# Kernel optimization log

Measured on AMD Instinct MI355X. Metric: run time of the kernel, lower is better.

Reference implementation:

```python
import jax, jax.numpy as jnp
import numpy as np

# SamplesLoss(loss='sinkhorn', p=1, blur=0.05): entropic regularization eps = blur**p = 0.05,
# debiased Sinkhorn divergence S(a,b) = OT(a,b) - 0.5*OT(a,a) - 0.5*OT(b,b).
EPS = 0.05
N_ITER = 50
N_POINTS = 32


def _cost(X, Y):
    # p=1 cost: Euclidean distance. X:[B,N,D] Y:[B,M,D] -> [B,N,M]
    d2 = jnp.sum((X[:, :, None, :] - Y[:, None, :, :]) ** 2, axis=-1)
    return jnp.sqrt(d2 + 1e-12)


def _ot(X, Y):
    # log-domain Sinkhorn with uniform weights; returns dual cost <mu,f>+<nu,g> per batch.
    B, N, _ = X.shape
    M = Y.shape[1]
    C = _cost(X, Y)  # [B,N,M]
    log_mu = jnp.full((B, N), -np.log(N), C.dtype)
    log_nu = jnp.full((B, M), -np.log(M), C.dtype)

    def body(carry, _):
        f, g = carry
        f = -EPS * jax.nn.logsumexp((g[:, None, :] - C) / EPS + log_nu[:, None, :], axis=2)
        g = -EPS * jax.nn.logsumexp((f[:, :, None] - C) / EPS + log_mu[:, :, None], axis=1)
        return (f, g), None

    init = (jnp.zeros((B, N), C.dtype), jnp.zeros((B, M), C.dtype))
    (f, g), _ = jax.lax.scan(body, init, None, length=N_ITER)
    return jnp.mean(f, axis=-1) + jnp.mean(g, axis=-1)  # uniform weights => mean


def _sinkhorn_div(X, Y):
    return _ot(X, Y) - 0.5 * _ot(X, X) - 0.5 * _ot(Y, Y)


def _encode(x, W, edge_index):
    # simple 1-layer GCN-style encoder: linear + mean neighbor aggregation + self, ReLU
    h = x @ W  # [n_nodes, emb_dim]
    src, dst = edge_index[0], edge_index[1]
    n = x.shape[0]
    agg = jax.ops.segment_sum(h[src], dst, num_segments=n)
    deg = jax.ops.segment_sum(jnp.ones(src.shape, h.dtype), dst, num_segments=n)
    return jax.nn.relu(h + agg / jnp.maximum(deg, 1.0)[:, None])


def setup_inputs() -> dict:
    key = jax.random.key(0)
    k1, k2, k3, k4, k5 = jax.random.split(key, 5)
    n_nodes, d_feat, emb_dim = 50000, 128, 256
    n_edges, n_pairs = 800000, 8192
    x = jax.random.normal(k1, (n_nodes, d_feat), jnp.float32)
    W = jax.random.normal(k2, (d_feat, emb_dim), jnp.float32) / np.sqrt(d_feat)
    edge_index = jax.random.randint(k3, (2, n_edges), 0, n_nodes, jnp.int64)
    pairs = jax.random.randint(k4, (2, n_pairs), 0, n_nodes, jnp.int64)
    graph_dist = jax.random.uniform(k5, (n_pairs,), jnp.float32, 1.0, 5.0)
    return {"x": x, "W": W, "edge_index": edge_index, "pairs": pairs,
            "graph_dist": graph_dist}


def reference(x, W, edge_index, pairs, graph_dist):
    z = _encode(x, W, edge_index)                       # [n_nodes, emb_dim]
    B = pairs.shape[1]
    Xa = z[pairs[0]].reshape(B, N_POINTS, -1)           # [B, n_points, space_dim]
    Xb = z[pairs[1]].reshape(B, N_POINTS, -1)
    distance = _sinkhorn_div(Xa, Xb)                    # = -score_pairs
    distortion = jnp.abs(distance - graph_dist) / graph_dist
    return jnp.mean(distortion)
```

## Files before the change

kernel.cpp:

```cpp
#include <hip/hip_runtime.h>

#define N_NODES 50000
#define N_EDGES 800000
#define N_PAIRS 8192
#define N_SLOTS (2 * N_PAIRS)
#define CAP     64

#define INV_EPS   20.0f
#define LOG2E_F   1.4426950408889634f
#define LN2_F     0.6931471805599453f
#define LN32_F    3.4657359027997265f
#define EPS_F     0.05f

typedef float f2 __attribute__((ext_vector_type(2)));

__global__ void k_mark(const int* __restrict__ pairs, int* __restrict__ flags) {
    int t = blockIdx.x * 256 + threadIdx.x;
    if (t < N_SLOTS) flags[pairs[t]] = 1;
}

__global__ __launch_bounds__(256) void k_scatter(
        const int* __restrict__ eidx, const int* __restrict__ flags,
        int* __restrict__ cnt, int* __restrict__ bucket) {
    int t = blockIdx.x * 256 + threadIdx.x;
    int dst = eidx[N_EDGES + t];
    if (!flags[dst]) return;
    int pos = atomicAdd(&cnt[dst], 1);
    if (pos < CAP) bucket[dst * CAP + pos] = eidx[t];
}

__global__ __launch_bounds__(256) void k_gemm(
        const int* __restrict__ pairs, const float* __restrict__ x,
        const int* __restrict__ cnt, const int* __restrict__ bucket,
        const float* __restrict__ W, float* __restrict__ Z) {
    __shared__ __align__(16) float Us[16 * 128];
    int sbase = blockIdx.x * 16;
    int t = threadIdx.x;
    int wave = t >> 6, lane = t & 63;

    #pragma unroll
    for (int rr = 0; rr < 4; ++rr) {
        int r = wave * 4 + rr;
        int node = pairs[sbase + r];
        int n = cnt[node];
        int m = (n < CAP) ? n : CAP;
        const int* bk = bucket + node * CAP;
        float ax = 0.0f, ay = 0.0f;
        int k = 0;
        for (; k + 4 <= m; k += 4) {
            int s0 = bk[k], s1 = bk[k + 1], s2 = bk[k + 2], s3 = bk[k + 3];
            float2 v0 = *(const float2*)(x + (size_t)s0 * 128 + lane * 2);
            float2 v1 = *(const float2*)(x + (size_t)s1 * 128 + lane * 2);
            float2 v2 = *(const float2*)(x + (size_t)s2 * 128 + lane * 2);
            float2 v3 = *(const float2*)(x + (size_t)s3 * 128 + lane * 2);
            ax += (v0.x + v1.x) + (v2.x + v3.x);
            ay += (v0.y + v1.y) + (v2.y + v3.y);
        }
        for (; k < m; ++k) {
            int s0 = bk[k];
            float2 v0 = *(const float2*)(x + (size_t)s0 * 128 + lane * 2);
            ax += v0.x;
            ay += v0.y;
        }
        float rdeg = 1.0f / fmaxf((float)n, 1.0f);
        float2 xv = *(const float2*)(x + (size_t)node * 128 + lane * 2);
        float2 o;
        o.x = fmaf(ax, rdeg, xv.x);
        o.y = fmaf(ay, rdeg, xv.y);
        *(float2*)(Us + r * 128 + lane * 2) = o;
    }
    __syncthreads();

    int jq = t & 63;
    int rq = t >> 6;
    float acc[4][4] = {};
    const float4* Wv = (const float4*)W;

    for (int k4 = 0; k4 < 32; ++k4) {
        float4 wv[4];
        #pragma unroll
        for (int i = 0; i < 4; ++i) wv[i] = Wv[(size_t)(k4 * 4 + i) * 64 + jq];
        #pragma unroll
        for (int r = 0; r < 4; ++r) {
            float4 uv = *(const float4*)(Us + (rq * 4 + r) * 128 + k4 * 4);
            float uk0 = uv.x, uk1 = uv.y, uk2 = uv.z, uk3 = uv.w;
            acc[r][0] = fmaf(uk0, wv[0].x, acc[r][0]);
            acc[r][1] = fmaf(uk0, wv[0].y, acc[r][1]);
            acc[r][2] = fmaf(uk0, wv[0].z, acc[r][2]);
            acc[r][3] = fmaf(uk0, wv[0].w, acc[r][3]);
            acc[r][0] = fmaf(uk1, wv[1].x, acc[r][0]);
            acc[r][1] = fmaf(uk1, wv[1].y, acc[r][1]);
            acc[r][2] = fmaf(uk1, wv[1].z, acc[r][2]);
            acc[r][3] = fmaf(uk1, wv[1].w, acc[r][3]);
            acc[r][0] = fmaf(uk2, wv[2].x, acc[r][0]);
            acc[r][1] = fmaf(uk2, wv[2].y, acc[r][1]);
            acc[r][2] = fmaf(uk2, wv[2].z, acc[r][2]);
            acc[r][3] = fmaf(uk2, wv[2].w, acc[r][3]);
            acc[r][0] = fmaf(uk3, wv[3].x, acc[r][0]);
            acc[r][1] = fmaf(uk3, wv[3].y, acc[r][1]);
            acc[r][2] = fmaf(uk3, wv[3].z, acc[r][2]);
            acc[r][3] = fmaf(uk3, wv[3].w, acc[r][3]);
        }
    }

    #pragma unroll
    for (int r = 0; r < 4; ++r) {
        float4 o;
        o.x = fmaxf(acc[r][0], 0.0f);
        o.y = fmaxf(acc[r][1], 0.0f);
        o.z = fmaxf(acc[r][2], 0.0f);
        o.w = fmaxf(acc[r][3], 0.0f);
        *(float4*)(Z + (size_t)(sbase + rq * 4 + r) * 256 + jq * 4) = o;
    }
}

__global__ __launch_bounds__(128) void k_sinkhorn(
        const float* __restrict__ Z, float* __restrict__ dist) {
    __shared__ __align__(16) float smem[2][640];

    int w = threadIdx.x >> 6;
    int lane = threadIdx.x & 63;
    const float CSCALE = -INV_EPS * LOG2E_F;
    const float CBIAS  = -LN32_F * LOG2E_F;

    if (blockIdx.x >= 4096) {
        float* sX = &smem[w][0];
        float* sY = &smem[w][256];
        float* sf = &smem[w][512];
        float* sg = &smem[w][544];
        float* su = &smem[w][576];
        float* sv = &smem[w][608];

        int b = (blockIdx.x - 4096) * 2 + w;
        int sx = b, sy = N_PAIRS + b;

        *(float4*)(&sX[lane * 4]) = ((const float4*)(Z + (size_t)sx * 256))[lane];
        *(float4*)(&sY[lane * 4]) = ((const float4*)(Z + (size_t)sy * 256))[lane];
        sg[lane & 31] = 0.0f;

        int i_r = lane & 31, jh = lane >> 5;
        int j_c = lane & 31, ih = lane >> 5;

        f2 CrowV[8], CcolV[8];
        {
            const f2* xp = (const f2*)(&sX[i_r * 8]);
            f2 x0 = xp[0], x1 = xp[1], x2 = xp[2], x3 = xp[3];
            #pragma unroll
            for (int t = 0; t < 16; ++t) {
                int j = jh * 16 + t;
                const f2* yp = (const f2*)(&sY[j * 8]);
                f2 d, s2;
                d = x0 - yp[0]; s2 = d * d;
                d = x1 - yp[1]; s2 = __builtin_elementwise_fma(d, d, s2);
                d = x2 - yp[2]; s2 = __builtin_elementwise_fma(d, d, s2);
                d = x3 - yp[3]; s2 = __builtin_elementwise_fma(d, d, s2);
                float d2 = s2.x + s2.y + 1e-12f;
                CrowV[t >> 1][t & 1] = fmaf(__builtin_amdgcn_sqrtf(d2), CSCALE, CBIAS);
            }
            const f2* yp = (const f2*)(&sY[j_c * 8]);
            f2 y0 = yp[0], y1 = yp[1], y2 = yp[2], y3 = yp[3];
            #pragma unroll
            for (int t = 0; t < 16; ++t) {
                int i = ih * 16 + t;
                const f2* qp = (const f2*)(&sX[i * 8]);
                f2 d, s2;
                d = qp[0] - y0; s2 = d * d;
                d = qp[1] - y1; s2 = __builtin_elementwise_fma(d, d, s2);
                d = qp[2] - y2; s2 = __builtin_elementwise_fma(d, d, s2);
                d = qp[3] - y3; s2 = __builtin_elementwise_fma(d, d, s2);
                float d2 = s2.x + s2.y + 1e-12f;
                CcolV[t >> 1][t & 1] = fmaf(__builtin_amdgcn_sqrtf(d2), CSCALE, CBIAS);
            }
        }

        float ft = 0.0f, gt = 0.0f;

        #pragma unroll 1
        for (int it = 0; it < 2; ++it) {
            {
                const float4* gp = (const float4*)(&sg[jh * 16]);
                float4 G0 = gp[0], G1 = gp[1], G2 = gp[2], G3 = gp[3];
                f2 gv[8] = {f2{G0.x, G0.y}, f2{G0.z, G0.w}, f2{G1.x, G1.y}, f2{G1.z, G1.w},
                            f2{G2.x, G2.y}, f2{G2.z, G2.w}, f2{G3.x, G3.y}, f2{G3.z, G3.w}};
                f2 val[8], m2 = f2{-1e30f, -1e30f};
                #pragma unroll
                for (int t2 = 0; t2 < 8; ++t2) {
                    val[t2] = gv[t2] + CrowV[t2];
                    m2 = __builtin_elementwise_max(m2, val[t2]);
                }
                float m = fmaxf(m2.x, m2.y);
                m = fmaxf(m, __shfl_xor(m, 32));
                f2 mm = f2{m, m};
                float s0 = 0.0f, s1 = 0.0f;
                #pragma unroll
                for (int t2 = 0; t2 < 8; ++t2) {
                    f2 e = val[t2] - mm;
                    s0 += __builtin_amdgcn_exp2f(e.x);
                    s1 += __builtin_amdgcn_exp2f(e.y);
                }
                float s = s0 + s1;
                s += __shfl_xor(s, 32);
                ft = -(m + __builtin_amdgcn_logf(s));
            }
            sf[lane & 31] = ft;
            {
                const float4* fp = (const float4*)(&sf[ih * 16]);
                float4 F0 = fp[0], F1 = fp[1], F2 = fp[2], F3 = fp[3];
                f2 fv[8] = {f2{F0.x, F0.y}, f2{F0.z, F0.w}, f2{F1.x, F1.y}, f2{F1.z, F1.w},
                            f2{F2.x, F2.y}, f2{F2.z, F2.w}, f2{F3.x, F3.y}, f2{F3.z, F3.w}};
                f2 val[8], m2 = f2{-1e30f, -1e30f};
                #pragma unroll
                for (int t2 = 0; t2 < 8; ++t2) {
                    val[t2] = fv[t2] + CcolV[t2];
                    m2 = __builtin_elementwise_max(m2, val[t2]);
                }
                float m = fmaxf(m2.x, m2.y);
                m = fmaxf(m, __shfl_xor(m, 32));
                f2 mm = f2{m, m};
                float s0 = 0.0f, s1 = 0.0f;
                #pragma unroll
                for (int t2 = 0; t2 < 8; ++t2) {
                    f2 e = val[t2] - mm;
                    s0 += __builtin_amdgcn_exp2f(e.x);
                    s1 += __builtin_amdgcn_exp2f(e.y);
                }
                float s = s0 + s1;
                s += __shfl_xor(s, 32);
                gt = -(m + __builtin_amdgcn_logf(s));
            }
            sg[lane & 31] = gt;
        }

        f2 KR2[8], KC2[8];
        float ureg = 1.0f, vreg = 1.0f;

        auto absorb = [&]() {
            const float4* gp = (const float4*)(&sg[jh * 16]);
            float4 G0 = gp[0], G1 = gp[1], G2 = gp[2], G3 = gp[3];
            f2 gv[8] = {f2{G0.x, G0.y}, f2{G0.z, G0.w}, f2{G1.x, G1.y}, f2{G1.z, G1.w},
                        f2{G2.x, G2.y}, f2{G2.z, G2.w}, f2{G3.x, G3.y}, f2{G3.z, G3.w}};
            f2 ftv = f2{ft, ft};
            #pragma unroll
            for (int t2 = 0; t2 < 8; ++t2) {
                f2 a = (gv[t2] + CrowV[t2]) + ftv;
                KR2[t2].x = __builtin_amdgcn_exp2f(a.x);
                KR2[t2].y = __builtin_amdgcn_exp2f(a.y);
            }
            const float4* fp = (const float4*)(&sf[ih * 16]);
            float4 F0 = fp[0], F1 = fp[1], F2 = fp[2], F3 = fp[3];
            f2 fv[8] = {f2{F0.x, F0.y}, f2{F0.z, F0.w}, f2{F1.x, F1.y}, f2{F1.z, F1.w},
                        f2{F2.x, F2.y}, f2{F2.z, F2.w}, f2{F3.x, F3.y}, f2{F3.z, F3.w}};
            f2 gtv = f2{gt, gt};
            #pragma unroll
            for (int t2 = 0; t2 < 8; ++t2) {
                f2 a = (fv[t2] + CcolV[t2]) + gtv;
                KC2[t2].x = __builtin_amdgcn_exp2f(a.x);
                KC2[t2].y = __builtin_amdgcn_exp2f(a.y);
            }
            sv[lane & 31] = 1.0f;
            ureg = 1.0f;
            vreg = 1.0f;
        };

        const int blens[5] = {6, 6, 12, 12, 12};
        absorb();
        #pragma unroll 1
        for (int blk = 0; blk < 5; ++blk) {
            int L = blens[blk];
            #pragma unroll 2
            for (int s6 = 0; s6 < L; ++s6) {
                {
                    const float4* vp = (const float4*)(&sv[jh * 16]);
                    float4 A0 = vp[0], A1 = vp[1], A2 = vp[2], A3 = vp[3];
                    f2 acc0 = KR2[0] * f2{A0.x, A0.y};
                    f2 acc1 = KR2[1] * f2{A0.z, A0.w};
                    acc0 = __builtin_elementwise_fma(KR2[2], f2{A1.x, A1.y}, acc0);
                    acc1 = __builtin_elementwise_fma(KR2[3], f2{A1.z, A1.w}, acc1);
                    acc0 = __builtin_elementwise_fma(KR2[4], f2{A2.x, A2.y}, acc0);
                    acc1 = __builtin_elementwise_fma(KR2[5], f2{A2.z, A2.w}, acc1);
                    acc0 = __builtin_elementwise_fma(KR2[6], f2{A3.x, A3.y}, acc0);
                    acc1 = __builtin_elementwise_fma(KR2[7], f2{A3.z, A3.w}, acc1);
                    f2 a = acc0 + acc1;
                    float S = a.x + a.y;
                    S += __shfl_xor(S, 32);
                    ureg = __builtin_amdgcn_rcpf(S);
                }
                su[lane & 31] = ureg;
                {
                    const float4* up = (const float4*)(&su[ih * 16]);
                    float4 A0 = up[0], A1 = up[1], A2 = up[2], A3 = up[3];
                    f2 acc0 = KC2[0] * f2{A0.x, A0.y};
                    f2 acc1 = KC2[1] * f2{A0.z, A0.w};
                    acc0 = __builtin_elementwise_fma(KC2[2], f2{A1.x, A1.y}, acc0);
                    acc1 = __builtin_elementwise_fma(KC2[3], f2{A1.z, A1.w}, acc1);
                    acc0 = __builtin_elementwise_fma(KC2[4], f2{A2.x, A2.y}, acc0);
                    acc1 = __builtin_elementwise_fma(KC2[5], f2{A2.z, A2.w}, acc1);
                    acc0 = __builtin_elementwise_fma(KC2[6], f2{A3.x, A3.y}, acc0);
                    acc1 = __builtin_elementwise_fma(KC2[7], f2{A3.z, A3.w}, acc1);
                    f2 a = acc0 + acc1;
                    float T = a.x + a.y;
                    T += __shfl_xor(T, 32);
                    vreg = __builtin_amdgcn_rcpf(T);
                }
                sv[lane & 31] = vreg;
            }
            if (blk < 4) {
                ft += __builtin_amdgcn_logf(ureg);
                gt += __builtin_amdgcn_logf(vreg);
                sf[lane & 31] = ft;
                sg[lane & 31] = gt;
                absorb();
            }
        }
        ft += __builtin_amdgcn_logf(ureg);
        gt += __builtin_amdgcn_logf(vreg);

        float v = ft + gt;
        #pragma unroll
        for (int off = 32; off > 0; off >>= 1) v += __shfl_xor(v, off);
        if (lane == 0) {
            float cost = v * (EPS_F * LN2_F / 64.0f);
            unsafeAtomicAdd(&dist[b], cost);
        }
    } else {
        int h = lane >> 5, i = lane & 31;
        int q = (i >> 4) & 1;
        int ip = i ^ 16;
        int P = blockIdx.x * 2 + w;
        int src = h ? (N_PAIRS + P) : P;

        float* sP  = &smem[w][h * 256];
        float* swv = &smem[w][512];
        float* spv = &smem[w][576];

        {
            const float4* zp = (const float4*)(Z + (size_t)src * 256);
            *(float4*)(&sP[i * 8])     = zp[i * 2];
            *(float4*)(&sP[i * 8 + 4]) = zp[i * 2 + 1];
        }

        f2 CA[8], CB[8];
        {
            const f2* xp = (const f2*)(&sP[i * 8]);
            f2 x0 = xp[0], x1 = xp[1], x2 = xp[2], x3 = xp[3];
            const f2* bp = (const f2*)(&sP[ip * 8]);
            f2 b0 = bp[0], b1 = bp[1], b2 = bp[2], b3 = bp[3];
            #pragma unroll
            for (int t = 0; t < 16; ++t) {
                int j = q * 16 + t;
                const f2* yp = (const f2*)(&sP[j * 8]);
                f2 y0 = yp[0], y1 = yp[1], y2 = yp[2], y3 = yp[3];
                f2 d, s2;
                d = x0 - y0; s2 = d * d;
                d = x1 - y1; s2 = __builtin_elementwise_fma(d, d, s2);
                d = x2 - y2; s2 = __builtin_elementwise_fma(d, d, s2);
                d = x3 - y3; s2 = __builtin_elementwise_fma(d, d, s2);
                float d2 = s2.x + s2.y + 1e-12f;
                CA[t >> 1][t & 1] = fmaf(__builtin_amdgcn_sqrtf(d2), CSCALE, CBIAS);
                d = b0 - y0; s2 = d * d;
                d = b1 - y1; s2 = __builtin_elementwise_fma(d, d, s2);
                d = b2 - y2; s2 = __builtin_elementwise_fma(d, d, s2);
                d = b3 - y3; s2 = __builtin_elementwise_fma(d, d, s2);
                float e2 = s2.x + s2.y + 1e-12f;
                CB[t >> 1][t & 1] = fmaf(__builtin_amdgcn_sqrtf(e2), CSCALE, CBIAS);
            }
        }

        float pp = 0.0f, E = 1.0f, wcur = 1.0f, wprev = 1.0f;
        f2 KA[8], KB[8];
        #pragma unroll
        for (int t = 0; t < 8; ++t) {
            KA[t].x = __builtin_amdgcn_exp2f(CA[t].x);
            KA[t].y = __builtin_amdgcn_exp2f(CA[t].y);
            KB[t].x = __builtin_amdgcn_exp2f(CB[t].x);
            KB[t].y = __builtin_amdgcn_exp2f(CB[t].y);
        }
        swv[lane] = 1.0f;

        const int blens[9] = {4, 12, 12, 12, 12, 12, 12, 12, 12};
        #pragma unroll 1
        for (int blk = 0; blk < 9; ++blk) {
            int L = blens[blk];
            #pragma unroll 2
            for (int s = 0; s < L; ++s) {
                const float4* wp = (const float4*)(&swv[h * 32 + q * 16]);
                float4 A0 = wp[0], A1 = wp[1], A2 = wp[2], A3 = wp[3];
                f2 aA0 = KA[0] * f2{A0.x, A0.y};
                f2 aA1 = KA[1] * f2{A0.z, A0.w};
                f2 aB0 = KB[0] * f2{A0.x, A0.y};
                f2 aB1 = KB[1] * f2{A0.z, A0.w};
                aA0 = __builtin_elementwise_fma(KA[2], f2{A1.x, A1.y}, aA0);
                aA1 = __builtin_elementwise_fma(KA[3], f2{A1.z, A1.w}, aA1);
                aB0 = __builtin_elementwise_fma(KB[2], f2{A1.x, A1.y}, aB0);
                aB1 = __builtin_elementwise_fma(KB[3], f2{A1.z, A1.w}, aB1);
                aA0 = __builtin_elementwise_fma(KA[4], f2{A2.x, A2.y}, aA0);
                aA1 = __builtin_elementwise_fma(KA[5], f2{A2.z, A2.w}, aA1);
                aB0 = __builtin_elementwise_fma(KB[4], f2{A2.x, A2.y}, aB0);
                aB1 = __builtin_elementwise_fma(KB[5], f2{A2.z, A2.w}, aB1);
                aA0 = __builtin_elementwise_fma(KA[6], f2{A3.x, A3.y}, aA0);
                aA1 = __builtin_elementwise_fma(KA[7], f2{A3.z, A3.w}, aA1);
                aB0 = __builtin_elementwise_fma(KB[6], f2{A3.x, A3.y}, aB0);
                aB1 = __builtin_elementwise_fma(KB[7], f2{A3.z, A3.w}, aB1);
                f2 aa = aA0 + aA1;
                f2 bb = aB0 + aB1;
                float pa = aa.x + aa.y;
                float pb = bb.x + bb.y;
                float other = __shfl_xor(pb, 16);
                float S = pa + other;
                wprev = wcur;
                wcur = __builtin_amdgcn_rcpf(S) * E;
                swv[h * 32 + i] = wcur;
            }
            if (blk < 8) {
                pp += __builtin_amdgcn_logf(wcur);
                spv[lane] = pp;
                const float4* pv = (const float4*)(&spv[h * 32 + q * 16]);
                float4 P0 = pv[0], P1 = pv[1], P2 = pv[2], P3 = pv[3];
                f2 pj[8] = {f2{P0.x,P0.y}, f2{P0.z,P0.w}, f2{P1.x,P1.y}, f2{P1.z,P1.w},
                            f2{P2.x,P2.y}, f2{P2.z,P2.w}, f2{P3.x,P3.y}, f2{P3.z,P3.w}};
                #pragma unroll
                for (int t = 0; t < 8; ++t) {
                    f2 a = pj[t] + CA[t];
                    KA[t].x = __builtin_amdgcn_exp2f(a.x);
                    KA[t].y = __builtin_amdgcn_exp2f(a.y);
                    f2 c = pj[t] + CB[t];
                    KB[t].x = __builtin_amdgcn_exp2f(c.x);
                    KB[t].y = __builtin_amdgcn_exp2f(c.y);
                }
                E = __builtin_amdgcn_exp2f(-pp);
                wcur = 1.0f;
                swv[lane] = 1.0f;
            }
        }

        float zsum = 2.0f * pp + __builtin_amdgcn_logf(wprev)
                   + __builtin_amdgcn_logf(wcur);
        #pragma unroll
        for (int off = 16; off > 0; off >>= 1) zsum += __shfl_xor(zsum, off);
        if (i == 0) {
            float cost = zsum * (EPS_F * LN2_F / 32.0f);
            unsafeAtomicAdd(&dist[P], -0.5f * cost);
        }
    }
}

__global__ void k_finalize(const float* __restrict__ dist,
                           const float* __restrict__ gd, float* __restrict__ out) {
    __shared__ float red[256];
    float s = 0.0f;
    for (int i = threadIdx.x; i < N_PAIRS; i += 256) {
        float g = gd[i];
        s += fabsf(dist[i] - g) / g;
    }
    red[threadIdx.x] = s;
    __syncthreads();
    for (int o = 128; o > 0; o >>= 1) {
        if (threadIdx.x < o) red[threadIdx.x] += red[threadIdx.x + o];
        __syncthreads();
    }
    if (threadIdx.x == 0) out[0] = red[0] * (1.0f / N_PAIRS);
}

extern "C" void kernel_launch(void* const* d_in, const int* in_sizes, int n_in,
                              void* d_out, int out_size, void* d_ws, size_t ws_size,
                              hipStream_t stream) {
    const float* x    = (const float*)d_in[0];
    const float* W    = (const float*)d_in[1];
    const int*   eidx = (const int*)d_in[2];
    const int*   pair = (const int*)d_in[3];
    const float* gd   = (const float*)d_in[4];

    char* ws = (char*)d_ws;
    size_t off = 0;
    int*   cnt    = (int*)  (ws + off); off += (size_t)N_NODES * 4;
    int*   flags  = (int*)  (ws + off); off += (size_t)N_NODES * 4;
    float* dist   = (float*)(ws + off); off += (size_t)N_PAIRS * 4;
    size_t zero_bytes = off;
    int*   bucket = (int*)  (ws + off); off += (size_t)N_NODES * CAP * 4;
    float* Z      = (float*)(ws + off); off += (size_t)N_SLOTS * 256 * 4;

    hipMemsetAsync(d_ws, 0, zero_bytes, stream);
    k_mark    <<<(N_SLOTS + 255) / 256, 256, 0, stream>>>(pair, flags);
    k_scatter <<<N_EDGES / 256, 256, 0, stream>>>(eidx, flags, cnt, bucket);
    k_gemm    <<<N_SLOTS / 16, 256, 0, stream>>>(pair, x, cnt, bucket, W, Z);
    k_sinkhorn<<<8192, 128, 0, stream>>>(Z, dist);
    k_finalize<<<1, 256, 0, stream>>>(dist, gd, (float*)d_out);
}
```

Baseline: 252.0 us.

## Interleave two Sinkhorn problems per wavefront and rescale kernels incrementally

Result: slower. 263.2 us (+4.4%).

```diff
diff --git a/kernel.cpp b/kernel.cpp
--- a/kernel.cpp
+++ b/kernel.cpp
@@ -114,233 +114,34 @@
     }
 }
 
-__global__ __launch_bounds__(128) void k_sinkhorn(
+__global__ __launch_bounds__(128, 4) void k_sinkhorn(
         const float* __restrict__ Z, float* __restrict__ dist) {
-    __shared__ __align__(16) float smem[2][640];
+    __shared__ __align__(16) float smem[2][1280];
 
     int w = threadIdx.x >> 6;
     int lane = threadIdx.x & 63;
+    float* S = &smem[w][0];
     const float CSCALE = -INV_EPS * LOG2E_F;
     const float CBIAS  = -LN32_F * LOG2E_F;
 
-    if (blockIdx.x >= 4096) {
-        float* sX = &smem[w][0];
-        float* sY = &smem[w][256];
-        float* sf = &smem[w][512];
-        float* sg = &smem[w][544];
-        float* su = &smem[w][576];
-        float* sv = &smem[w][608];
-
-        int b = (blockIdx.x - 4096) * 2 + w;
-        int sx = b, sy = N_PAIRS + b;
-
-        *(float4*)(&sX[lane * 4]) = ((const float4*)(Z + (size_t)sx * 256))[lane];
-        *(float4*)(&sY[lane * 4]) = ((const float4*)(Z + (size_t)sy * 256))[lane];
-        sg[lane & 31] = 0.0f;
-
-        int i_r = lane & 31, jh = lane >> 5;
-        int j_c = lane & 31, ih = lane >> 5;
-
-        f2 CrowV[8], CcolV[8];
-        {
-            const f2* xp = (const f2*)(&sX[i_r * 8]);
-            f2 x0 = xp[0], x1 = xp[1], x2 = xp[2], x3 = xp[3];
-            #pragma unroll
-            for (int t = 0; t < 16; ++t) {
-                int j = jh * 16 + t;
-                const f2* yp = (const f2*)(&sY[j * 8]);
-                f2 d, s2;
-                d = x0 - yp[0]; s2 = d * d;
-                d = x1 - yp[1]; s2 = __builtin_elementwise_fma(d, d, s2);
-                d = x2 - yp[2]; s2 = __builtin_elementwise_fma(d, d, s2);
-                d = x3 - yp[3]; s2 = __builtin_elementwise_fma(d, d, s2);
-                float d2 = s2.x + s2.y + 1e-12f;
-                CrowV[t >> 1][t & 1] = fmaf(__builtin_amdgcn_sqrtf(d2), CSCALE, CBIAS);
-            }
-            const f2* yp = (const f2*)(&sY[j_c * 8]);
-            f2 y0 = yp[0], y1 = yp[1], y2 = yp[2], y3 = yp[3];
-            #pragma unroll
-            for (int t = 0; t < 16; ++t) {
-                int i = ih * 16 + t;
-                const f2* qp = (const f2*)(&sX[i * 8]);
-                f2 d, s2;
-                d = qp[0] - y0; s2 = d * d;
-                d = qp[1] - y1; s2 = __builtin_elementwise_fma(d, d, s2);
-                d = qp[2] - y2; s2 = __builtin_elementwise_fma(d, d, s2);
-                d = qp[3] - y3; s2 = __builtin_elementwise_fma(d, d, s2);
-                float d2 = s2.x + s2.y + 1e-12f;
-                CcolV[t >> 1][t & 1] = fmaf(__builtin_amdgcn_sqrtf(d2), CSCALE, CBIAS);
-            }
-        }
-
-        float ft = 0.0f, gt = 0.0f;
-
-        #pragma unroll 1
-        for (int it = 0; it < 2; ++it) {
-            {
-                const float4* gp = (const float4*)(&sg[jh * 16]);
-                float4 G0 = gp[0], G1 = gp[1], G2 = gp[2], G3 = gp[3];
-                f2 gv[8] = {f2{G0.x, G0.y}, f2{G0.z, G0.w}, f2{G1.x, G1.y}, f2{G1.z, G1.w},
-                            f2{G2.x, G2.y}, f2{G2.z, G2.w}, f2{G3.x, G3.y}, f2{G3.z, G3.w}};
-                f2 val[8], m2 = f2{-1e30f, -1e30f};
-                #pragma unroll
-                for (int t2 = 0; t2 < 8; ++t2) {
-                    val[t2] = gv[t2] + CrowV[t2];
-                    m2 = __builtin_elementwise_max(m2, val[t2]);
-                }
-                float m = fmaxf(m2.x, m2.y);
-                m = fmaxf(m, __shfl_xor(m, 32));
-                f2 mm = f2{m, m};
-                float s0 = 0.0f, s1 = 0.0f;
-                #pragma unroll
-                for (int t2 = 0; t2 < 8; ++t2) {
-                    f2 e = val[t2] - mm;
-                    s0 += __builtin_amdgcn_exp2f(e.x);
-                    s1 += __builtin_amdgcn_exp2f(e.y);
-                }
-                float s = s0 + s1;
-                s += __shfl_xor(s, 32);
-                ft = -(m + __builtin_amdgcn_logf(s));
-            }
-            sf[lane & 31] = ft;
-            {
-                const float4* fp = (const float4*)(&sf[ih * 16]);
-                float4 F0 = fp[0], F1 = fp[1], F2 = fp[2], F3 = fp[3];
-                f2 fv[8] = {f2{F0.x, F0.y}, f2{F0.z, F0.w}, f2{F1.x, F1.y}, f2{F1.z, F1.w},
-                            f2{F2.x, F2.y}, f2{F2.z, F2.w}, f2{F3.x, F3.y}, f2{F3.z, F3.w}};
-                f2 val[8], m2 = f2{-1e30f, -1e30f};
-                #pragma unroll
-                for (int t2 = 0; t2 < 8; ++t2) {
-                    val[t2] = fv[t2] + CcolV[t2];
-                    m2 = __builtin_elementwise_max(m2, val[t2]);
-                }
-                float m = fmaxf(m2.x, m2.y);
-                m = fmaxf(m, __shfl_xor(m, 32));
-                f2 mm = f2{m, m};
-                float s0 = 0.0f, s1 = 0.0f;
-                #pragma unroll
-                for (int t2 = 0; t2 < 8; ++t2) {
-                    f2 e = val[t2] - mm;
-                    s0 += __builtin_amdgcn_exp2f(e.x);
-                    s1 += __builtin_amdgcn_exp2f(e.y);
-                }
-                float s = s0 + s1;
-                s += __shfl_xor(s, 32);
-                gt = -(m + __builtin_amdgcn_logf(s));
-            }
-            sg[lane & 31] = gt;
-        }
-
-        f2 KR2[8], KC2[8];
-        float ureg = 1.0f, vreg = 1.0f;
-
-        auto absorb = [&]() {
-            const float4* gp = (const float4*)(&sg[jh * 16]);
-            float4 G0 = gp[0], G1 = gp[1], G2 = gp[2], G3 = gp[3];
-            f2 gv[8] = {f2{G0.x, G0.y}, f2{G0.z, G0.w}, f2{G1.x, G1.y}, f2{G1.z, G1.w},
-                        f2{G2.x, G2.y}, f2{G2.z, G2.w}, f2{G3.x, G3.y}, f2{G3.z, G3.w}};
-            f2 ftv = f2{ft, ft};
-            #pragma unroll
-            for (int t2 = 0; t2 < 8; ++t2) {
-                f2 a = (gv[t2] + CrowV[t2]) + ftv;
-                KR2[t2].x = __builtin_amdgcn_exp2f(a.x);
-                KR2[t2].y = __builtin_amdgcn_exp2f(a.y);
-            }
-            const float4* fp = (const float4*)(&sf[ih * 16]);
-            float4 F0 = fp[0], F1 = fp[1], F2 = fp[2], F3 = fp[3];
-            f2 fv[8] = {f2{F0.x, F0.y}, f2{F0.z, F0.w}, f2{F1.x, F1.y}, f2{F1.z, F1.w},
-                        f2{F2.x, F2.y}, f2{F2.z, F2.w}, f2{F3.x, F3.y}, f2{F3.z, F3.w}};
-            f2 gtv = f2{gt, gt};
-            #pragma unroll
-            for (int t2 = 0; t2 < 8; ++t2) {
-                f2 a = (fv[t2] + CcolV[t2]) + gtv;
-                KC2[t2].x = __builtin_amdgcn_exp2f(a.x);
-                KC2[t2].y = __builtin_amdgcn_exp2f(a.y);
-            }
-            sv[lane & 31] = 1.0f;
-            ureg = 1.0f;
-            vreg = 1.0f;
-        };
-
-        const int blens[5] = {6, 6, 12, 12, 12};
-        absorb();
-        #pragma unroll 1
-        for (int blk = 0; blk < 5; ++blk) {
-            int L = blens[blk];
-            #pragma unroll 2
-            for (int s6 = 0; s6 < L; ++s6) {
-                {
-                    const float4* vp = (const float4*)(&sv[jh * 16]);
-                    float4 A0 = vp[0], A1 = vp[1], A2 = vp[2], A3 = vp[3];
-                    f2 acc0 = KR2[0] * f2{A0.x, A0.y};
-                    f2 acc1 = KR2[1] * f2{A0.z, A0.w};
-                    acc0 = __builtin_elementwise_fma(KR2[2], f2{A1.x, A1.y}, acc0);
-                    acc1 = __builtin_elementwise_fma(KR2[3], f2{A1.z, A1.w}, acc1);
-                    acc0 = __builtin_elementwise_fma(KR2[4], f2{A2.x, A2.y}, acc0);
-                    acc1 = __builtin_elementwise_fma(KR2[5], f2{A2.z, A2.w}, acc1);
-                    acc0 = __builtin_elementwise_fma(KR2[6], f2{A3.x, A3.y}, acc0);
-                    acc1 = __builtin_elementwise_fma(KR2[7], f2{A3.z, A3.w}, acc1);
-                    f2 a = acc0 + acc1;
-                    float S = a.x + a.y;
-                    S += __shfl_xor(S, 32);
-                    ureg = __builtin_amdgcn_rcpf(S);
-                }
-                su[lane & 31] = ureg;
-                {
-                    const float4* up = (const float4*)(&su[ih * 16]);
-                    float4 A0 = up[0], A1 = up[1], A2 = up[2], A3 = up[3];
-                    f2 acc0 = KC2[0] * f2{A0.x, A0.y};
-                    f2 acc1 = KC2[1] * f2{A0.z, A0.w};
-                    acc0 = __builtin_elementwise_fma(KC2[2], f2{A1.x, A1.y}, acc0);
-                    acc1 = __builtin_elementwise_fma(KC2[3], f2{A1.z, A1.w}, acc1);
-                    acc0 = __builtin_elementwise_fma(KC2[4], f2{A2.x, A2.y}, acc0);
-                    acc1 = __builtin_elementwise_fma(KC2[5], f2{A2.z, A2.w}, acc1);
-                    acc0 = __builtin_elementwise_fma(KC2[6], f2{A3.x, A3.y}, acc0);
-                    acc1 = __builtin_elementwise_fma(KC2[7], f2{A3.z, A3.w}, acc1);
-                    f2 a = acc0 + acc1;
-                    float T = a.x + a.y;
-                    T += __shfl_xor(T, 32);
-                    vreg = __builtin_amdgcn_rcpf(T);
-                }
-                sv[lane & 31] = vreg;
-            }
-            if (blk < 4) {
-                ft += __builtin_amdgcn_logf(ureg);
-                gt += __builtin_amdgcn_logf(vreg);
-                sf[lane & 31] = ft;
-                sg[lane & 31] = gt;
-                absorb();
-            }
-        }
-        ft += __builtin_amdgcn_logf(ureg);
-        gt += __builtin_amdgcn_logf(vreg);
-
-        float v = ft + gt;
-        #pragma unroll
-        for (int off = 32; off > 0; off >>= 1) v += __shfl_xor(v, off);
-        if (lane == 0) {
-            float cost = v * (EPS_F * LN2_F / 64.0f);
-            unsafeAtomicAdd(&dist[b], cost);
-        }
-    } else {
+    if (blockIdx.x < 2048) {
         int h = lane >> 5, i = lane & 31;
         int q = (i >> 4) & 1;
         int ip = i ^ 16;
-        int P = blockIdx.x * 2 + w;
-        int src = h ? (N_PAIRS + P) : P;
-
-        float* sP  = &smem[w][h * 256];
-        float* swv = &smem[w][512];
-        float* spv = &smem[w][576];
-
-        {
+        int Pb = blockIdx.x * 4 + w * 2;
+
+        f2 KA[2][8], KB[2][8];
+        float pp[2] = {0.0f, 0.0f}, E[2] = {1.0f, 1.0f};
+        float wcur[2] = {1.0f, 1.0f}, wprev[2] = {1.0f, 1.0f};
+
+        #pragma unroll
+        for (int tk = 0; tk < 2; ++tk) {
+            int P = Pb + tk;
+            int src = h ? (N_PAIRS + P) : P;
+            float* sP = S + tk * 512 + h * 256;
             const float4* zp = (const float4*)(Z + (size_t)src * 256);
             *(float4*)(&sP[i * 8])     = zp[i * 2];
             *(float4*)(&sP[i * 8 + 4]) = zp[i * 2 + 1];
-        }
-
-        f2 CA[8], CB[8];
-        {
             const f2* xp = (const f2*)(&sP[i * 8]);
             f2 x0 = xp[0], x1 = xp[1], x2 = xp[2], x3 = xp[3];
             const f2* bp = (const f2*)(&sP[ip * 8]);
@@ -356,90 +157,368 @@
                 d = x2 - y2; s2 = __builtin_elementwise_fma(d, d, s2);
                 d = x3 - y3; s2 = __builtin_elementwise_fma(d, d, s2);
                 float d2 = s2.x + s2.y + 1e-12f;
-                CA[t >> 1][t & 1] = fmaf(__builtin_amdgcn_sqrtf(d2), CSCALE, CBIAS);
+                KA[tk][t >> 1][t & 1] = __builtin_amdgcn_exp2f(
+                    fmaf(__builtin_amdgcn_sqrtf(d2), CSCALE, CBIAS));
                 d = b0 - y0; s2 = d * d;
                 d = b1 - y1; s2 = __builtin_elementwise_fma(d, d, s2);
                 d = b2 - y2; s2 = __builtin_elementwise_fma(d, d, s2);
                 d = b3 - y3; s2 = __builtin_elementwise_fma(d, d, s2);
                 float e2 = s2.x + s2.y + 1e-12f;
-                CB[t >> 1][t & 1] = fmaf(__builtin_amdgcn_sqrtf(e2), CSCALE, CBIAS);
-            }
-        }
-
-        float pp = 0.0f, E = 1.0f, wcur = 1.0f, wprev = 1.0f;
-        f2 KA[8], KB[8];
-        #pragma unroll
-        for (int t = 0; t < 8; ++t) {
-            KA[t].x = __builtin_amdgcn_exp2f(CA[t].x);
-            KA[t].y = __builtin_amdgcn_exp2f(CA[t].y);
-            KB[t].x = __builtin_amdgcn_exp2f(CB[t].x);
-            KB[t].y = __builtin_amdgcn_exp2f(CB[t].y);
-        }
-        swv[lane] = 1.0f;
+                KB[tk][t >> 1][t & 1] = __builtin_amdgcn_exp2f(
+                    fmaf(__builtin_amdgcn_sqrtf(e2), CSCALE, CBIAS));
+            }
+            (S + 1024 + tk * 64)[lane] = 1.0f;
+        }
 
         const int blens[9] = {4, 12, 12, 12, 12, 12, 12, 12, 12};
         #pragma unroll 1
         for (int blk = 0; blk < 9; ++blk) {
             int L = blens[blk];
-            #pragma unroll 2
+            #pragma unroll 1
             for (int s = 0; s < L; ++s) {
-                const float4* wp = (const float4*)(&swv[h * 32 + q * 16]);
-                float4 A0 = wp[0], A1 = wp[1], A2 = wp[2], A3 = wp[3];
-                f2 aA0 = KA[0] * f2{A0.x, A0.y};
-                f2 aA1 = KA[1] * f2{A0.z, A0.w};
-                f2 aB0 = KB[0] * f2{A0.x, A0.y};
-                f2 aB1 = KB[1] * f2{A0.z, A0.w};
-                aA0 = __builtin_elementwise_fma(KA[2], f2{A1.x, A1.y}, aA0);
-                aA1 = __builtin_elementwise_fma(KA[3], f2{A1.z, A1.w}, aA1);
-                aB0 = __builtin_elementwise_fma(KB[2], f2{A1.x, A1.y}, aB0);
-                aB1 = __builtin_elementwise_fma(KB[3], f2{A1.z, A1.w}, aB1);
-                aA0 = __builtin_elementwise_fma(KA[4], f2{A2.x, A2.y}, aA0);
-                aA1 = __builtin_elementwise_fma(KA[5], f2{A2.z, A2.w}, aA1);
-                aB0 = __builtin_elementwise_fma(KB[4], f2{A2.x, A2.y}, aB0);
-                aB1 = __builtin_elementwise_fma(KB[5], f2{A2.z, A2.w}, aB1);
-                aA0 = __builtin_elementwise_fma(KA[6], f2{A3.x, A3.y}, aA0);
-                aA1 = __builtin_elementwise_fma(KA[7], f2{A3.z, A3.w}, aA1);
-                aB0 = __builtin_elementwise_fma(KB[6], f2{A3.x, A3.y}, aB0);
-                aB1 = __builtin_elementwise_fma(KB[7], f2{A3.z, A3.w}, aB1);
-                f2 aa = aA0 + aA1;
-                f2 bb = aB0 + aB1;
-                float pa = aa.x + aa.y;
-                float pb = bb.x + bb.y;
-                float other = __shfl_xor(pb, 16);
-                float S = pa + other;
-                wprev = wcur;
-                wcur = __builtin_amdgcn_rcpf(S) * E;
-                swv[h * 32 + i] = wcur;
+                #pragma unroll
+                for (int tk = 0; tk < 2; ++tk) {
+                    float* swv = S + 1024 + tk * 64;
+                    const float4* wp = (const float4*)(&swv[h * 32 + q * 16]);
+                    float4 A0 = wp[0], A1 = wp[1], A2 = wp[2], A3 = wp[3];
+                    f2 aA0 = KA[tk][0] * f2{A0.x, A0.y};
+                    f2 aA1 = KA[tk][1] * f2{A0.z, A0.w};
+                    f2 aB0 = KB[tk][0] * f2{A0.x, A0.y};
+                    f2 aB1 = KB[tk][1] * f2{A0.z, A0.w};
+                    aA0 = __builtin_elementwise_fma(KA[tk][2], f2{A1.x, A1.y}, aA0);
+                    aA1 = __builtin_elementwise_fma(KA[tk][3], f2{A1.z, A1.w}, aA1);
+                    aB0 = __builtin_elementwise_fma(KB[tk][2], f2{A1.x, A1.y}, aB0);
+                    aB1 = __builtin_elementwise_fma(KB[tk][3], f2{A1.z, A1.w}, aB1);
+                    aA0 = __builtin_elementwise_fma(KA[tk][4], f2{A2.x, A2.y}, aA0);
+                    aA1 = __builtin_elementwise_fma(KA[tk][5], f2{A2.z, A2.w}, aA1);
+                    aB0 = __builtin_elementwise_fma(KB[tk][4], f2{A2.x, A2.y}, aB0);
+                    aB1 = __builtin_elementwise_fma(KB[tk][5], f2{A2.z, A2.w}, aB1);
+                    aA0 = __builtin_elementwise_fma(KA[tk][6], f2{A3.x, A3.y}, aA0);
+                    aA1 = __builtin_elementwise_fma(KA[tk][7], f2{A3.z, A3.w}, aA1);
+                    aB0 = __builtin_elementwise_fma(KB[tk][6], f2{A3.x, A3.y}, aB0);
+                    aB1 = __builtin_elementwise_fma(KB[tk][7], f2{A3.z, A3.w}, aB1);
+                    f2 aa = aA0 + aA1;
+                    f2 bb = aB0 + aB1;
+                    float pa = aa.x + aa.y;
+                    float pb = bb.x + bb.y;
+                    float other = __shfl_xor(pb, 16);
+                    float Sv = pa + other;
+                    wprev[tk] = wcur[tk];
+                    wcur[tk] = __builtin_amdgcn_rcpf(Sv) * E[tk];
+                    swv[h * 32 + i] = wcur[tk];
+                }
             }
             if (blk < 8) {
-                pp += __builtin_amdgcn_logf(wcur);
-                spv[lane] = pp;
-                const float4* pv = (const float4*)(&spv[h * 32 + q * 16]);
-                float4 P0 = pv[0], P1 = pv[1], P2 = pv[2], P3 = pv[3];
-                f2 pj[8] = {f2{P0.x,P0.y}, f2{P0.z,P0.w}, f2{P1.x,P1.y}, f2{P1.z,P1.w},
-                            f2{P2.x,P2.y}, f2{P2.z,P2.w}, f2{P3.x,P3.y}, f2{P3.z,P3.w}};
-                #pragma unroll
-                for (int t = 0; t < 8; ++t) {
-                    f2 a = pj[t] + CA[t];
-                    KA[t].x = __builtin_amdgcn_exp2f(a.x);
-                    KA[t].y = __builtin_amdgcn_exp2f(a.y);
-                    f2 c = pj[t] + CB[t];
-                    KB[t].x = __builtin_amdgcn_exp2f(c.x);
-                    KB[t].y = __builtin_amdgcn_exp2f(c.y);
-                }
-                E = __builtin_amdgcn_exp2f(-pp);
-                wcur = 1.0f;
-                swv[lane] = 1.0f;
-            }
-        }
-
-        float zsum = 2.0f * pp + __builtin_amdgcn_logf(wprev)
-                   + __builtin_amdgcn_logf(wcur);
+                #pragma unroll
+                for (int tk = 0; tk < 2; ++tk) {
+                    float* swv = S + 1024 + tk * 64;
+                    float* sdp = S + 1152 + tk * 64;
+                    float d = __builtin_amdgcn_logf(wcur[tk]);
+                    pp[tk] += d;
+                    sdp[h * 32 + i] = d;
+                    const float4* dv = (const float4*)(&sdp[h * 32 + q * 16]);
+                    float4 D0 = dv[0], D1 = dv[1], D2 = dv[2], D3 = dv[3];
+                    float ex[16];
+                    ex[0] = __builtin_amdgcn_exp2f(D0.x);
+                    ex[1] = __builtin_amdgcn_exp2f(D0.y);
+                    ex[2] = __builtin_amdgcn_exp2f(D0.z);
+                    ex[3] = __builtin_amdgcn_exp2f(D0.w);
+                    ex[4] = __builtin_amdgcn_exp2f(D1.x);
+                    ex[5] = __builtin_amdgcn_exp2f(D1.y);
+                    ex[6] = __builtin_amdgcn_exp2f(D1.z);
+                    ex[7] = __builtin_amdgcn_exp2f(D1.w);
+                    ex[8] = __builtin_amdgcn_exp2f(D2.x);
+                    ex[9] = __builtin_amdgcn_exp2f(D2.y);
+                    ex[10] = __builtin_amdgcn_exp2f(D2.z);
+                    ex[11] = __builtin_amdgcn_exp2f(D2.w);
+                    ex[12] = __builtin_amdgcn_exp2f(D3.x);
+                    ex[13] = __builtin_amdgcn_exp2f(D3.y);
+                    ex[14] = __builtin_amdgcn_exp2f(D3.z);
+                    ex[15] = __builtin_amdgcn_exp2f(D3.w);
+                    #pragma unroll
+                    for (int t2 = 0; t2 < 8; ++t2) {
+                        f2 ee = f2{ex[2 * t2], ex[2 * t2 + 1]};
+                        KA[tk][t2] *= ee;
+                        KB[tk][t2] *= ee;
+                    }
+                    E[tk] = __builtin_amdgcn_exp2f(-pp[tk]);
+                    wcur[tk] = 1.0f;
+                    swv[lane] = 1.0f;
+                }
+            }
+        }
+
         #pragma unroll
-        for (int off = 16; off > 0; off >>= 1) zsum += __shfl_xor(zsum, off);
-        if (i == 0) {
-            float cost = zsum * (EPS_F * LN2_F / 32.0f);
-            unsafeAtomicAdd(&dist[P], -0.5f * cost);
+        for (int tk = 0; tk < 2; ++tk) {
+            float zsum = 2.0f * pp[tk] + __builtin_amdgcn_logf(wprev[tk])
+                       + __builtin_amdgcn_logf(wcur[tk]);
+            #pragma unroll
+            for (int off = 16; off > 0; off >>= 1) zsum += __shfl_xor(zsum, off);
+            if (i == 0) {
+                float cost = zsum * (EPS_F * LN2_F / 32.0f);
+                unsafeAtomicAdd(&dist[Pb + tk], -0.5f * cost);
+            }
+        }
+    } else {
+        int jh = lane >> 5;
+        int ih = lane >> 5;
+        int i_r = lane & 31;
+        int Bb = (blockIdx.x - 2048) * 4 + w * 2;
+
+        f2 KR[2][8], KC[2][8];
+        float ftA[2], gtA[2];
+        float ureg[2] = {1.0f, 1.0f}, vreg[2] = {1.0f, 1.0f};
+
+        #pragma unroll 1
+        for (int tk = 0; tk < 2; ++tk) {
+            int b = Bb + tk;
+            float* sX = S + tk * 512;
+            float* sY = sX + 256;
+            float* sf = S + 1024 + tk * 128;
+            float* sg = sf + 32;
+            float* sv = sf + 96;
+            *(float4*)(&sX[lane * 4]) = ((const float4*)(Z + (size_t)b * 256))[lane];
+            *(float4*)(&sY[lane * 4]) = ((const float4*)(Z + (size_t)(N_PAIRS + b) * 256))[lane];
+            sg[i_r] = 0.0f;
+
+            f2 CrowV[8], CcolV[8];
+            {
+                const f2* xp = (const f2*)(&sX[i_r * 8]);
+                f2 x0 = xp[0], x1 = xp[1], x2 = xp[2], x3 = xp[3];
+                #pragma unroll
+                for (int t = 0; t < 16; ++t) {
+                    int j = jh * 16 + t;
+                    const f2* yp = (const f2*)(&sY[j * 8]);
+                    f2 d, s2;
+                    d = x0 - yp[0]; s2 = d * d;
+                    d = x1 - yp[1]; s2 = __builtin_elementwise_fma(d, d, s2);
+                    d = x2 - yp[2]; s2 = __builtin_elementwise_fma(d, d, s2);
+                    d = x3 - yp[3]; s2 = __builtin_elementwise_fma(d, d, s2);
+                    float d2 = s2.x + s2.y + 1e-12f;
+                    CrowV[t >> 1][t & 1] = fmaf(__builtin_amdgcn_sqrtf(d2), CSCALE, CBIAS);
+                }
+                const f2* yp = (const f2*)(&sY[i_r * 8]);
+                f2 y0 = yp[0], y1 = yp[1], y2 = yp[2], y3 = yp[3];
+                #pragma unroll
+                for (int t = 0; t < 16; ++t) {
+                    int i = ih * 16 + t;
+                    const f2* qp = (const f2*)(&sX[i * 8]);
+                    f2 d, s2;
+                    d = qp[0] - y0; s2 = d * d;
+                    d = qp[1] - y1; s2 = __builtin_elementwise_fma(d, d, s2);
+                    d = qp[2] - y2; s2 = __builtin_elementwise_fma(d, d, s2);
+                    d = qp[3] - y3; s2 = __builtin_elementwise_fma(d, d, s2);
+                    float d2 = s2.x + s2.y + 1e-12f;
+                    CcolV[t >> 1][t & 1] = fmaf(__builtin_amdgcn_sqrtf(d2), CSCALE, CBIAS);
+                }
+            }
+
+            float ft = 0.0f, gt = 0.0f;
+            #pragma unroll 1
+            for (int it = 0; it < 2; ++it) {
+                {
+                    const float4* gp = (const float4*)(&sg[jh * 16]);
+                    float4 G0 = gp[0], G1 = gp[1], G2 = gp[2], G3 = gp[3];
+                    f2 gv[8] = {f2{G0.x, G0.y}, f2{G0.z, G0.w}, f2{G1.x, G1.y}, f2{G1.z, G1.w},
+                                f2{G2.x, G2.y}, f2{G2.z, G2.w}, f2{G3.x, G3.y}, f2{G3.z, G3.w}};
+                    f2 val[8], m2 = f2{-1e30f, -1e30f};
+                    #pragma unroll
+                    for (int t2 = 0; t2 < 8; ++t2) {
+                        val[t2] = gv[t2] + CrowV[t2];
+                        m2 = __builtin_elementwise_max(m2, val[t2]);
+                    }
+                    float m = fmaxf(m2.x, m2.y);
+                    m = fmaxf(m, __shfl_xor(m, 32));
+                    f2 mm = f2{m, m};
+                    float s0 = 0.0f, s1 = 0.0f;
+                    #pragma unroll
+                    for (int t2 = 0; t2 < 8; ++t2) {
+                        f2 e = val[t2] - mm;
+                        s0 += __builtin_amdgcn_exp2f(e.x);
+                        s1 += __builtin_amdgcn_exp2f(e.y);
+                    }
+                    float s = s0 + s1;
+                    s += __shfl_xor(s, 32);
+                    ft = -(m + __builtin_amdgcn_logf(s));
+                }
+                sf[i_r] = ft;
+                {
+                    const float4* fp = (const float4*)(&sf[ih * 16]);
+                    float4 F0 = fp[0], F1 = fp[1], F2 = fp[2], F3 = fp[3];
+                    f2 fv[8] = {f2{F0.x, F0.y}, f2{F0.z, F0.w}, f2{F1.x, F1.y}, f2{F1.z, F1.w},
+                                f2{F2.x, F2.y}, f2{F2.z, F2.w}, f2{F3.x, F3.y}, f2{F3.z, F3.w}};
+                    f2 val[8], m2 = f2{-1e30f, -1e30f};
+                    #pragma unroll
+                    for (int t2 = 0; t2 < 8; ++t2) {
+                        val[t2] = fv[t2] + CcolV[t2];
+                        m2 = __builtin_elementwise_max(m2, val[t2]);
+                    }
+                    float m = fmaxf(m2.x, m2.y);
+                    m = fmaxf(m, __shfl_xor(m, 32));
+                    f2 mm = f2{m, m};
+                    float s0 = 0.0f, s1 = 0.0f;
+                    #pragma unroll
+                    for (int t2 = 0; t2 < 8; ++t2) {
+                        f2 e = val[t2] - mm;
+                        s0 += __builtin_amdgcn_exp2f(e.x);
+                        s1 += __builtin_amdgcn_exp2f(e.y);
+                    }
+                    float s = s0 + s1;
+                    s += __shfl_xor(s, 32);
+                    gt = -(m + __builtin_amdgcn_logf(s));
+                }
+                sg[i_r] = gt;
+            }
+
+            {
+                const float4* gp = (const float4*)(&sg[jh * 16]);
+                float4 G0 = gp[0], G1 = gp[1], G2 = gp[2], G3 = gp[3];
+                f2 gv[8] = {f2{G0.x, G0.y}, f2{G0.z, G0.w}, f2{G1.x, G1.y}, f2{G1.z, G1.w},
+                            f2{G2.x, G2.y}, f2{G2.z, G2.w}, f2{G3.x, G3.y}, f2{G3.z, G3.w}};
+                f2 ftv = f2{ft, ft};
+                #pragma unroll
+                for (int t2 = 0; t2 < 8; ++t2) {
+                    f2 a = (gv[t2] + CrowV[t2]) + ftv;
+                    KR[tk][t2].x = __builtin_amdgcn_exp2f(a.x);
+                    KR[tk][t2].y = __builtin_amdgcn_exp2f(a.y);
+                }
+                const float4* fp = (const float4*)(&sf[ih * 16]);
+                float4 F0 = fp[0], F1 = fp[1], F2 = fp[2], F3 = fp[3];
+                f2 fv[8] = {f2{F0.x, F0.y}, f2{F0.z, F0.w}, f2{F1.x, F1.y}, f2{F1.z, F1.w},
+                            f2{F2.x, F2.y}, f2{F2.z, F2.w}, f2{F3.x, F3.y}, f2{F3.z, F3.w}};
+                f2 gtv = f2{gt, gt};
+                #pragma unroll
+                for (int t2 = 0; t2 < 8; ++t2) {
+                    f2 a = (fv[t2] + CcolV[t2]) + gtv;
+                    KC[tk][t2].x = __builtin_amdgcn_exp2f(a.x);
+                    KC[tk][t2].y = __builtin_amdgcn_exp2f(a.y);
+                }
+            }
+            sv[i_r] = 1.0f;
+            ftA[tk] = ft;
+            gtA[tk] = gt;
+        }
+
+        const int blens[5] = {6, 6, 12, 12, 12};
+        #pragma unroll 1
+        for (int blk = 0; blk < 5; ++blk) {
+            int L = blens[blk];
+            #pragma unroll 1
+            for (int s6 = 0; s6 < L; ++s6) {
+                #pragma unroll
+                for (int tk = 0; tk < 2; ++tk) {
+                    float* su = S + 1024 + tk * 128 + 64;
+                    float* sv = su + 32;
+                    const float4* vp = (const float4*)(&sv[jh * 16]);
+                    float4 A0 = vp[0], A1 = vp[1], A2 = vp[2], A3 = vp[3];
+                    f2 acc0 = KR[tk][0] * f2{A0.x, A0.y};
+                    f2 acc1 = KR[tk][1] * f2{A0.z, A0.w};
+                    acc0 = __builtin_elementwise_fma(KR[tk][2], f2{A1.x, A1.y}, acc0);
+                    acc1 = __builtin_elementwise_fma(KR[tk][3], f2{A1.z, A1.w}, acc1);
+                    acc0 = __builtin_elementwise_fma(KR[tk][4], f2{A2.x, A2.y}, acc0);
+                    acc1 = __builtin_elementwise_fma(KR[tk][5], f2{A2.z, A2.w}, acc1);
+                    acc0 = __builtin_elementwise_fma(KR[tk][6], f2{A3.x, A3.y}, acc0);
+                    acc1 = __builtin_elementwise_fma(KR[tk][7], f2{A3.z, A3.w}, acc1);
+                    f2 a = acc0 + acc1;
+                    float Sv = a.x + a.y;
+                    Sv += __shfl_xor(Sv, 32);
+                    ureg[tk] = __builtin_amdgcn_rcpf(Sv);
+                    su[i_r] = ureg[tk];
+                }
+                #pragma unroll
+                for (int tk = 0; tk < 2; ++tk) {
+                    float* su = S + 1024 + tk * 128 + 64;
+                    float* sv = su + 32;
+                    const float4* up = (const float4*)(&su[ih * 16]);
+                    float4 A0 = up[0], A1 = up[1], A2 = up[2], A3 = up[3];
+                    f2 acc0 = KC[tk][0] * f2{A0.x, A0.y};
+                    f2 acc1 = KC[tk][1] * f2{A0.z, A0.w};
+                    acc0 = __builtin_elementwise_fma(KC[tk][2], f2{A1.x, A1.y}, acc0);
+                    acc1 = __builtin_elementwise_fma(KC[tk][3], f2{A1.z, A1.w}, acc1);
+                    acc0 = __builtin_elementwise_fma(KC[tk][4], f2{A2.x, A2.y}, acc0);
+                    acc1 = __builtin_elementwise_fma(KC[tk][5], f2{A2.z, A2.w}, acc1);
+                    acc0 = __builtin_elementwise_fma(KC[tk][6], f2{A3.x, A3.y}, acc0);
+                    acc1 = __builtin_elementwise_fma(KC[tk][7], f2{A3.z, A3.w}, acc1);
+                    f2 a = acc0 + acc1;
+                    float Tv = a.x + a.y;
+                    Tv += __shfl_xor(Tv, 32);
+                    vreg[tk] = __builtin_amdgcn_rcpf(Tv);
+                    sv[i_r] = vreg[tk];
+                }
+            }
+            if (blk < 4) {
+                #pragma unroll
+                for (int tk = 0; tk < 2; ++tk) {
+                    float* sf = S + 1024 + tk * 128;
+                    float* sg = sf + 32;
+                    float* sv = sf + 96;
+                    float df = __builtin_amdgcn_logf(ureg[tk]);
+                    float dg = __builtin_amdgcn_logf(vreg[tk]);
+                    ftA[tk] += df;
+                    gtA[tk] += dg;
+                    sf[i_r] = df;
+                    sg[i_r] = dg;
+                    const float4* dgv = (const float4*)(&sg[jh * 16]);
+                    float4 D0 = dgv[0], D1 = dgv[1], D2 = dgv[2], D3 = dgv[3];
+                    float ex[16];
+                    ex[0] = __builtin_amdgcn_exp2f(df + D0.x);
+                    ex[1] = __builtin_amdgcn_exp2f(df + D0.y);
+                    ex[2] = __builtin_amdgcn_exp2f(df + D0.z);
+                    ex[3] = __builtin_amdgcn_exp2f(df + D0.w);
+                    ex[4] = __builtin_amdgcn_exp2f(df + D1.x);
+                    ex[5] = __builtin_amdgcn_exp2f(df + D1.y);
+                    ex[6] = __builtin_amdgcn_exp2f(df + D1.z);
+                    ex[7] = __builtin_amdgcn_exp2f(df + D1.w);
+                    ex[8] = __builtin_amdgcn_exp2f(df + D2.x);
+                    ex[9] = __builtin_amdgcn_exp2f(df + D2.y);
+                    ex[10] = __builtin_amdgcn_exp2f(df + D2.z);
+                    ex[11] = __builtin_amdgcn_exp2f(df + D2.w);
+                    ex[12] = __builtin_amdgcn_exp2f(df + D3.x);
+                    ex[13] = __builtin_amdgcn_exp2f(df + D3.y);
+                    ex[14] = __builtin_amdgcn_exp2f(df + D3.z);
+                    ex[15] = __builtin_amdgcn_exp2f(df + D3.w);
+                    #pragma unroll
+                    for (int t2 = 0; t2 < 8; ++t2)
+                        KR[tk][t2] *= f2{ex[2 * t2], ex[2 * t2 + 1]};
+                    const float4* dfv = (const float4*)(&sf[ih * 16]);
+                    float4 E0 = dfv[0], E1 = dfv[1], E2 = dfv[2], E3 = dfv[3];
+                    ex[0] = __builtin_amdgcn_exp2f(dg + E0.x);
+                    ex[1] = __builtin_amdgcn_exp2f(dg + E0.y);
+                    ex[2] = __builtin_amdgcn_exp2f(dg + E0.z);
+                    ex[3] = __builtin_amdgcn_exp2f(dg + E0.w);
+                    ex[4] = __builtin_amdgcn_exp2f(dg + E1.x);
+                    ex[5] = __builtin_amdgcn_exp2f(dg + E1.y);
+                    ex[6] = __builtin_amdgcn_exp2f(dg + E1.z);
+                    ex[7] = __builtin_amdgcn_exp2f(dg + E1.w);
+                    ex[8] = __builtin_amdgcn_exp2f(dg + E2.x);
+                    ex[9] = __builtin_amdgcn_exp2f(dg + E2.y);
+                    ex[10] = __builtin_amdgcn_exp2f(dg + E2.z);
+                    ex[11] = __builtin_amdgcn_exp2f(dg + E2.w);
+                    ex[12] = __builtin_amdgcn_exp2f(dg + E3.x);
+                    ex[13] = __builtin_amdgcn_exp2f(dg + E3.y);
+                    ex[14] = __builtin_amdgcn_exp2f(dg + E3.z);
+                    ex[15] = __builtin_amdgcn_exp2f(dg + E3.w);
+                    #pragma unroll
+                    for (int t2 = 0; t2 < 8; ++t2)
+                        KC[tk][t2] *= f2{ex[2 * t2], ex[2 * t2 + 1]};
+                    sv[i_r] = 1.0f;
+                    ureg[tk] = 1.0f;
+                    vreg[tk] = 1.0f;
+                }
+            }
+        }
+
+        #pragma unroll
+        for (int tk = 0; tk < 2; ++tk) {
+            float ft = ftA[tk] + __builtin_amdgcn_logf(ureg[tk]);
+            float gt = gtA[tk] + __builtin_amdgcn_logf(vreg[tk]);
+            float v = ft + gt;
+            #pragma unroll
+            for (int off = 32; off > 0; off >>= 1) v += __shfl_xor(v, off);
+            if (lane == 0) {
+                float cost = v * (EPS_F * LN2_F / 64.0f);
+                unsafeAtomicAdd(&dist[Bb + tk], cost);
+            }
         }
     }
 }
@@ -483,6 +562,6 @@
     k_mark    <<<(N_SLOTS + 255) / 256, 256, 0, stream>>>(pair, flags);
     k_scatter <<<N_EDGES / 256, 256, 0, stream>>>(eidx, flags, cnt, bucket);
     k_gemm    <<<N_SLOTS / 16, 256, 0, stream>>>(pair, x, cnt, bucket, W, Z);
-    k_sinkhorn<<<8192, 128, 0, stream>>>(Z, dist);
+    k_sinkhorn<<<4096, 128, 0, stream>>>(Z, dist);
     k_finalize<<<1, 256, 0, stream>>>(dist, gd, (float*)d_out);
 }
```
